# Kernel optimization log

Measured on AMD Instinct MI355X. Metric: run time of the kernel, lower is better.

## Reference

```python
import jax, jax.numpy as jnp
import numpy as np

N = 100000   # nodes
E = 1000000  # edges
F_IN = 64    # input node features
EMB = 32     # init_emb
C = 32       # hidden/out channels per head
H = 4        # heads
HC = H * C   # 128
NEG_SLOPE = 0.2


def setup_inputs() -> dict:
    key = jax.random.key(0)
    ks = jax.random.split(key, 40)
    g = lambda k, shape: jax.random.normal(k, shape, jnp.float32) * 0.05
    inp = {
        "x": jax.random.normal(ks[0], (N, F_IN), jnp.float32),
        "edge_index": jax.random.randint(ks[1], (2, E), 0, N, jnp.int32),
        "W0": g(ks[2], (F_IN, EMB)),
    }
    i = 3
    for p, din in (("f", EMB), ("m", HC), ("l", HC)):
        inp[p + "_Wl"] = g(ks[i], (din, HC)); i += 1
        inp[p + "_bl"] = g(ks[i], (HC,));     i += 1
        inp[p + "_Wr"] = g(ks[i], (din, HC)); i += 1
        inp[p + "_br"] = g(ks[i], (HC,));     i += 1
        inp[p + "_att"] = g(ks[i], (H, C));   i += 1
        inp[p + "_cb"] = g(ks[i], (HC,));     i += 1
        inp[p + "_Ws"] = g(ks[i], (din, HC)); i += 1
        inp[p + "_bs"] = g(ks[i], (HC,));     i += 1
    return inp


def _gatv2(x, src, dst, Wl, bl, Wr, br, att, cb):
    # GATv2Conv, bipartite weights, concat heads, add_self_loops=False
    xl = (x @ Wl + bl).reshape(-1, H, C)  # source transform [N,H,C]
    xr = (x @ Wr + br).reshape(-1, H, C)  # target transform [N,H,C]
    e = xl[src] + xr[dst]                 # [E,H,C]
    s = jnp.where(e > 0, e, NEG_SLOPE * e)
    score = jnp.einsum('ehc,hc->eh', s, att)  # [E,H]
    mmax = jax.ops.segment_max(score, dst, num_segments=N)
    ex = jnp.exp(score - mmax[dst])
    den = jax.ops.segment_sum(ex, dst, num_segments=N)
    alpha = ex / den[dst]                 # segment softmax over in-edges
    out = jax.ops.segment_sum(xl[src] * alpha[:, :, None], dst, num_segments=N)
    return out.reshape(-1, HC) + cb


def reference(x, edge_index,
              W0,
              f_Wl, f_bl, f_Wr, f_br, f_att, f_cb, f_Ws, f_bs,
              m_Wl, m_bl, m_Wr, m_br, m_att, m_cb, m_Ws, m_bs,
              l_Wl, l_bl, l_Wr, l_br, l_att, l_cb, l_Ws, l_bs):
    src, dst = edge_index[0], edge_index[1]
    h = jax.nn.relu(x @ W0)
    h = jax.nn.relu(_gatv2(h, src, dst, f_Wl, f_bl, f_Wr, f_br, f_att, f_cb) + h @ f_Ws + f_bs)
    for _ in range(3):  # conv_mid / lin_mid weights are SHARED across the 3 iterations
        h = jax.nn.relu(_gatv2(h, src, dst, m_Wl, m_bl, m_Wr, m_br, m_att, m_cb) + h @ m_Ws + m_bs)
    h = _gatv2(h, src, dst, l_Wl, l_bl, l_Wr, l_br, l_att, l_cb) + h @ l_Ws + l_bs
    h = h / jnp.linalg.norm(h, axis=-1, keepdims=True)
    return h
```

## Files before the change

### kernel.cpp

```cpp
#include <hip/hip_runtime.h>
#include <hip/hip_bf16.h>
#include <math.h>

#define N_NODES 100000
#define N_EDGES 1000000
#define NEG_SLOPE 0.2f
#define NBUCK 98
#define BSHIFT 10
#define SLAB 12288
#define BINA_EDGES 4096

typedef short v8s __attribute__((ext_vector_type(8)));
typedef float v4f __attribute__((ext_vector_type(4)));

__device__ inline unsigned pack_bf16(float a, float b) {
    unsigned ua = __float_as_uint(a);
    unsigned ub = __float_as_uint(b);
    ua = (ua + 0x7FFFu + ((ua >> 16) & 1u)) >> 16;
    ub = (ub + 0x7FFFu + ((ub >> 16) & 1u)) >> 16;
    return ua | (ub << 16);
}
__device__ inline unsigned short bf16_rn(float x) {
    unsigned u = __float_as_uint(x);
    u = (u + 0x7FFFu + ((u >> 16) & 1u)) >> 16;
    return (unsigned short)u;
}
__device__ inline void unpack8(uint4 u, float* f) {
    f[0] = __uint_as_float(u.x << 16); f[1] = __uint_as_float(u.x & 0xFFFF0000u);
    f[2] = __uint_as_float(u.y << 16); f[3] = __uint_as_float(u.y & 0xFFFF0000u);
    f[4] = __uint_as_float(u.z << 16); f[5] = __uint_as_float(u.z & 0xFFFF0000u);
    f[6] = __uint_as_float(u.w << 16); f[7] = __uint_as_float(u.w & 0xFFFF0000u);
}

__global__ void init_cursors(int* __restrict__ gcursor) {
    int t = blockIdx.x * blockDim.x + threadIdx.x;
    if (t < NBUCK) gcursor[t] = t * SLAB;
}

__global__ __launch_bounds__(256) void binA_kernel(
    const int* __restrict__ src, const int* __restrict__ dst,
    int* __restrict__ gcursor, int* __restrict__ tmp) {
    __shared__ int bstart[NBUCK];
    __shared__ int addrbase[NBUCK];
    __shared__ int bcur[NBUCK];
    __shared__ int s[256];
    __shared__ int staged_val[BINA_EDGES];
    __shared__ int staged_addr[BINA_EDGES];
    const int tid = threadIdx.x;
    const int base = blockIdx.x * BINA_EDGES;
    const int ecount = min(BINA_EDGES, N_EDGES - base);

    if (tid < NBUCK) bcur[tid] = 0;
    __syncthreads();
    for (int j = tid; j < ecount; j += 256) {
        int d = dst[base + j];
        atomicAdd(&bcur[d >> BSHIFT], 1);
    }
    __syncthreads();
    int own = (tid < NBUCK) ? bcur[tid] : 0;
    s[tid] = own;
    __syncthreads();
    for (int off = 1; off < 256; off <<= 1) {
        int u = (tid >= off) ? s[tid - off] : 0;
        __syncthreads();
        s[tid] += u;
        __syncthreads();
    }
    if (tid < NBUCK) {
        int excl = s[tid] - own;
        bstart[tid] = excl;
        int resv = atomicAdd(&gcursor[tid], own);
        addrbase[tid] = resv - excl;
    }
    __syncthreads();
    if (tid < NBUCK) bcur[tid] = bstart[tid];
    __syncthreads();
    for (int j = tid; j < ecount; j += 256) {
        int d = dst[base + j];
        int sr = src[base + j];
        int bk = d >> BSHIFT;
        int lpos = atomicAdd(&bcur[bk], 1);
        staged_val[lpos] = ((d & ((1 << BSHIFT) - 1)) << 17) | sr;
        staged_addr[lpos] = addrbase[bk] + lpos;
    }
    __syncthreads();
    for (int j = tid; j < ecount; j += 256)
        tmp[staged_addr[j]] = staged_val[j];
}

__global__ void bucket_scan(const int* __restrict__ gcursor, int* __restrict__ bbase,
                            int* __restrict__ row_ptr) {
    __shared__ int s[128];
    int t = threadIdx.x;
    int v = (t < NBUCK) ? (gcursor[t] - t * SLAB) : 0;
    s[t] = v;
    __syncthreads();
    for (int off = 1; off < 128; off <<= 1) {
        int u = (t >= off) ? s[t - off] : 0;
        __syncthreads();
        s[t] += u;
        __syncthreads();
    }
    if (t < NBUCK) bbase[t] = s[t] - v;
    if (t == 0) row_ptr[N_NODES] = N_EDGES;
}

__global__ __launch_bounds__(256) void binB_kernel(
    const int* __restrict__ tmp, const int* __restrict__ gcursor,
    const int* __restrict__ bbase, int* __restrict__ row_ptr,
    int* __restrict__ srcs) {
    __shared__ int hist[1024];
    __shared__ int tsum[256];
    const int b = blockIdx.x;
    const int tid = threadIdx.x;
    const int base = b * SLAB;
    const int cnt = gcursor[b] - base;
    const int node0 = b << BSHIFT;
    const int nodes_in = min(1024, N_NODES - node0);
    const int gb = bbase[b];

    for (int i = tid; i < 1024; i += 256) hist[i] = 0;
    __syncthreads();
    for (int i = tid; i < cnt; i += 256)
        atomicAdd(&hist[tmp[base + i] >> 17], 1);
    __syncthreads();
    int v[4], local = 0;
#pragma unroll
    for (int j = 0; j < 4; ++j) {
        v[j] = hist[tid * 4 + j];
        local += v[j];
    }
    tsum[tid] = local;
    __syncthreads();
    for (int off = 1; off < 256; off <<= 1) {
        int u = (tid >= off) ? tsum[tid - off] : 0;
        __syncthreads();
        tsum[tid] += u;
        __syncthreads();
    }
    int run = tsum[tid] - local;
#pragma unroll
    for (int j = 0; j < 4; ++j) {
        hist[tid * 4 + j] = run;
        run += v[j];
    }
    __syncthreads();
    for (int i = tid; i < nodes_in; i += 256)
        row_ptr[node0 + i] = gb + hist[i];
    __syncthreads();
    for (int i = tid; i < cnt; i += 256) {
        int e = tmp[base + i];
        int pos = atomicAdd(&hist[e >> 17], 1);
        srcs[gb + pos] = e & 0x1FFFF;
    }
}

template <int K>
__global__ void convert_w(const float* __restrict__ Wl, const float* __restrict__ Wr,
                          const float* __restrict__ Ws, unsigned short* __restrict__ wt) {
    int idx = blockIdx.x * blockDim.x + threadIdx.x;
    if (idx >= 384 * K) return;
    int n = idx / K;
    int k = idx - n * K;
    int sec = n >> 7;
    int nn = n & 127;
    const float* W = (sec == 0) ? Wl : (sec == 1) ? Wr : Ws;
    wt[idx] = bf16_rn(W[k * 128 + nn]);
}

__global__ void h0_kernel(const float* __restrict__ x, const float* __restrict__ W0,
                          unsigned short* __restrict__ h) {
    int tid = blockIdx.x * blockDim.x + threadIdx.x;
    int col = tid & 31;
    int row = tid >> 5;
    if (row >= N_NODES) return;
    const float* xr = x + row * 64;
    float acc = 0.f;
#pragma unroll
    for (int k = 0; k < 64; ++k) acc = fmaf(xr[k], W0[k * 32 + col], acc);
    h[row * 32 + col] = bf16_rn(fmaxf(acc, 0.f));
}

template <int K>
__global__ __launch_bounds__(64) void mm3_mfma(
    const unsigned short* __restrict__ A, const unsigned short* __restrict__ Wt,
    const float* __restrict__ bl, const float* __restrict__ br, const float* __restrict__ bs,
    const float* __restrict__ cb,
    unsigned short* __restrict__ xl_bf, unsigned short* __restrict__ xr_bf,
    unsigned short* __restrict__ sk_bf) {
    const int lane = threadIdx.x & 63;
    const int q = lane >> 4;
    const int li = lane & 15;
    const int r0 = blockIdx.x * 64;
    constexpr int KS = K / 32;

    v8s a[4][KS];
#pragma unroll
    for (int mi = 0; mi < 4; ++mi) {
        int row = r0 + mi * 16 + li;
        row = row < N_NODES ? row : N_NODES - 1;
#pragma unroll
        for (int ks = 0; ks < KS; ++ks)
            a[mi][ks] = *(const v8s*)&A[(size_t)row * K + ks * 32 + q * 8];
    }

    for (int t = 0; t < 6; ++t) {
        const int sec = t >> 1;
        const int c0 = (t & 1) * 64;
        v4f acc[4][4];
#pragma unroll
        for (int mi = 0; mi < 4; ++mi)
#pragma unroll
            for (int ni = 0; ni < 4; ++ni) acc[mi][ni] = (v4f)(0.f);

#pragma unroll
        for (int ks = 0; ks < KS; ++ks) {
            v8s b[4];
#pragma unroll
            for (int ni = 0; ni < 4; ++ni) {
                int col = sec * 128 + c0 + ni * 16 + li;
                b[ni] = *(const v8s*)&Wt[(size_t)col * K + ks * 32 + q * 8];
            }
#pragma unroll
            for (int mi = 0; mi < 4; ++mi)
#pragma unroll
                for (int ni = 0; ni < 4; ++ni)
                    acc[mi][ni] = __builtin_amdgcn_mfma_f32_16x16x32_bf16(b[ni], a[mi][ks], acc[mi][ni], 0, 0, 0);
        }

        unsigned short* dstp = (sec == 0) ? xl_bf : (sec == 1) ? xr_bf : sk_bf;
#pragma unroll
        for (int ni = 0; ni < 4; ++ni) {
            int cbase = c0 + ni * 16 + q * 4;
            float4 b4;
            if (sec == 0) b4 = *(const float4*)&bl[cbase];
            else if (sec == 1) b4 = *(const float4*)&br[cbase];
            else {
                float4 t1 = *(const float4*)&bs[cbase];
                float4 t2 = *(const float4*)&cb[cbase];
                b4 = make_float4(t1.x + t2.x, t1.y + t2.y, t1.z + t2.z, t1.w + t2.w);
            }
#pragma unroll
            for (int mi = 0; mi < 4; ++mi) {
                int row = r0 + mi * 16 + li;
                if (row >= N_NODES) continue;
                v4f v = acc[mi][ni];
                uint2 pk;
                pk.x = pack_bf16(v[0] + b4.x, v[1] + b4.y);
                pk.y = pack_bf16(v[2] + b4.z, v[3] + b4.w);
                *(uint2*)&dstp[(size_t)row * 128 + cbase] = pk;
            }
        }
    }
}

#define AGG_BODY(XC, SVC, CB)                                               \
    {                                                                       \
        float xf[8];                                                        \
        unpack8(XC, xf);                                                    \
        bool vld = (CB) + g < end;                                          \
        if ((CB) + 12 < end) XC = xlb4[(size_t)SVC * 16 + li];              \
        if ((CB) + 24 < end) {                                              \
            int ii = (CB) + 24 + g;                                         \
            SVC = srcs[ii < end ? ii : em1];                                \
        }                                                                   \
        float p1 = 0.f, p2 = 0.f;                                           \
        _Pragma("unroll") for (int i = 0; i < 8; ++i) {                     \
            float e_ = xf[i] + xr_f[i];                                     \
            p1 = fmaf(e_, at_f[i], p1);                                     \
            p2 = fmaf(fabsf(e_), at_f[i], p2);                              \
        }                                                                   \
        float p = fmaf(0.6f, p1, 0.4f * p2);                                \
        p += __shfl_xor(p, 1);                                              \
        p += __shfl_xor(p, 2);                                              \
        float w = vld ? __expf(p) : 0.f;                                    \
        lsum += w;                                                          \
        _Pragma("unroll") for (int i = 0; i < 8; ++i)                       \
            acc[i] = fmaf(xf[i], w, acc[i]);                                \
    }

__global__ __launch_bounds__(256, 7) void agg_kernel(
    const uint4* __restrict__ xlb4, const uint4* __restrict__ xrb4,
    const uint4* __restrict__ skb4, const int* __restrict__ row_ptr,
    const int* __restrict__ srcs, const float* __restrict__ att,
    uint4* __restrict__ out_bf, float* __restrict__ out_f,
    int write_bf, int do_relu, int do_norm) {
    int n = (blockIdx.x * blockDim.x + threadIdx.x) >> 6;
    if (n >= N_NODES) return;
    int lane = threadIdx.x & 63;
    int g = lane >> 4, li = lane & 15;

    const int beg = __builtin_amdgcn_readfirstlane(row_ptr[n]);
    const int end = __builtin_amdgcn_readfirstlane(row_ptr[n + 1]);

    uint4 xru = xrb4[(size_t)n * 16 + li];
    uint4 sku = skb4[(size_t)n * 16 + li];

    float at_f[8];
    *(float4*)&at_f[0] = *(const float4*)&att[li * 8];
    *(float4*)&at_f[4] = *(const float4*)&att[li * 8 + 4];
    float xr_f[8];
    unpack8(xru, xr_f);

    float acc[8];
#pragma unroll
    for (int i = 0; i < 8; ++i) acc[i] = 0.f;
    float lsum = 0.f;

    if (beg < end) {
        const int em1 = end - 1;
#define SRC_AT(Q) ({ int _ii = beg + (Q) * 4 + g; srcs[_ii < end ? _ii : em1]; })
        int sv0 = SRC_AT(0), sv1 = SRC_AT(1), sv2 = SRC_AT(2);
        uint4 x0 = xlb4[(size_t)sv0 * 16 + li];
        uint4 x1 = xlb4[(size_t)sv1 * 16 + li];
        uint4 x2 = xlb4[(size_t)sv2 * 16 + li];
        sv0 = SRC_AT(3);
        sv1 = SRC_AT(4);
        sv2 = SRC_AT(5);
#undef SRC_AT

        for (int cb = beg; cb < end; cb += 12) {
            AGG_BODY(x0, sv0, cb)
            if (cb + 4 < end) AGG_BODY(x1, sv1, cb + 4)
            if (cb + 8 < end) AGG_BODY(x2, sv2, cb + 8)
        }
    }

#pragma unroll
    for (int i = 0; i < 8; ++i) {
        acc[i] += __shfl_xor(acc[i], 16);
        acc[i] += __shfl_xor(acc[i], 32);
    }
    lsum += __shfl_xor(lsum, 16);
    lsum += __shfl_xor(lsum, 32);

    float inv = (lsum > 0.f) ? 1.f / lsum : 0.f;
    float sk_f[8];
    unpack8(sku, sk_f);
    float o[8];
#pragma unroll
    for (int i = 0; i < 8; ++i) o[i] = fmaf(acc[i], inv, sk_f[i]);
    if (do_relu) {
#pragma unroll
        for (int i = 0; i < 8; ++i) o[i] = fmaxf(o[i], 0.f);
    }
    if (do_norm) {
        float ss = 0.f;
#pragma unroll
        for (int i = 0; i < 8; ++i) ss = fmaf(o[i], o[i], ss);
        ss += __shfl_xor(ss, 1);
        ss += __shfl_xor(ss, 2);
        ss += __shfl_xor(ss, 4);
        ss += __shfl_xor(ss, 8);
        float r = 1.0f / sqrtf(ss);
#pragma unroll
        for (int i = 0; i < 8; ++i) o[i] *= r;
    }
    if (g == 0) {
        if (write_bf) {
            uint4 pk;
            pk.x = pack_bf16(o[0], o[1]);
            pk.y = pack_bf16(o[2], o[3]);
            pk.z = pack_bf16(o[4], o[5]);
            pk.w = pack_bf16(o[6], o[7]);
            out_bf[(size_t)n * 16 + li] = pk;
        } else {
            *(float4*)&out_f[(size_t)n * 128 + li * 8] = make_float4(o[0], o[1], o[2], o[3]);
            *(float4*)&out_f[(size_t)n * 128 + li * 8 + 4] = make_float4(o[4], o[5], o[6], o[7]);
        }
    }
}

extern "C" void kernel_launch(void* const* d_in, const int* in_sizes, int n_in,
                              void* d_out, int out_size, void* d_ws, size_t ws_size,
                              hipStream_t stream) {
    const float* x = (const float*)d_in[0];
    const int* ei = (const int*)d_in[1];
    const int* src = ei;
    const int* dst = ei + N_EDGES;
    const float* W0 = (const float*)d_in[2];

    const float* f_p[8];
    const float* m_p[8];
    const float* l_p[8];
    for (int i = 0; i < 8; ++i) f_p[i] = (const float*)d_in[3 + i];
    for (int i = 0; i < 8; ++i) m_p[i] = (const float*)d_in[11 + i];
    for (int i = 0; i < 8; ++i) l_p[i] = (const float*)d_in[19 + i];

    char* ws = (char*)d_ws;
    unsigned short* xl_bf = (unsigned short*)ws; ws += (size_t)N_NODES * 128 * 2;
    unsigned short* xr_bf = (unsigned short*)ws; ws += (size_t)N_NODES * 128 * 2;
    unsigned short* sk_bf = (unsigned short*)ws; ws += (size_t)N_NODES * 128 * 2;
    unsigned short* h_bf = (unsigned short*)ws;  ws += (size_t)N_NODES * 128 * 2;
    int* row_ptr = (int*)ws;       ws += (size_t)(N_NODES + 1) * 4;
    int* srcs = (int*)ws;          ws += (size_t)N_EDGES * 4;
    int* tmp = (int*)ws;           ws += (size_t)NBUCK * SLAB * 4;
    int* gcursor = (int*)ws;       ws += (size_t)NBUCK * 4;
    int* bbase = (int*)ws;         ws += (size_t)NBUCK * 4;
    unsigned short* wt_f = (unsigned short*)ws; ws += (size_t)384 * 32 * 2;
    unsigned short* wt_m = (unsigned short*)ws; ws += (size_t)384 * 128 * 2;
    unsigned short* wt_l = (unsigned short*)ws; ws += (size_t)384 * 128 * 2;

    init_cursors<<<1, 128, 0, stream>>>(gcursor);
    binA_kernel<<<(N_EDGES + BINA_EDGES - 1) / BINA_EDGES, 256, 0, stream>>>(src, dst, gcursor, tmp);
    bucket_scan<<<1, 128, 0, stream>>>(gcursor, bbase, row_ptr);
    binB_kernel<<<NBUCK, 256, 0, stream>>>(tmp, gcursor, bbase, row_ptr, srcs);

    convert_w<32><<<(384 * 32 + 255) / 256, 256, 0, stream>>>(f_p[0], f_p[2], f_p[6], wt_f);
    convert_w<128><<<(384 * 128 + 255) / 256, 256, 0, stream>>>(m_p[0], m_p[2], m_p[6], wt_m);
    convert_w<128><<<(384 * 128 + 255) / 256, 256, 0, stream>>>(l_p[0], l_p[2], l_p[6], wt_l);

    h0_kernel<<<(N_NODES * 32) / 256, 256, 0, stream>>>(x, W0, h_bf);

    const int gmm = (N_NODES + 63) / 64;
    const int gagg = (N_NODES * 64) / 256;
    float* out = (float*)d_out;

    mm3_mfma<32><<<gmm, 64, 0, stream>>>(h_bf, wt_f, f_p[1], f_p[3], f_p[7], f_p[5],
                                         xl_bf, xr_bf, sk_bf);
    agg_kernel<<<gagg, 256, 0, stream>>>((uint4*)xl_bf, (uint4*)xr_bf, (uint4*)sk_bf,
                                         row_ptr, srcs, f_p[4],
                                         (uint4*)h_bf, nullptr, 1, 1, 0);

    for (int it = 0; it < 3; ++it) {
        mm3_mfma<128><<<gmm, 64, 0, stream>>>(h_bf, wt_m, m_p[1], m_p[3], m_p[7], m_p[5],
                                              xl_bf, xr_bf, sk_bf);
        agg_kernel<<<gagg, 256, 0, stream>>>((uint4*)xl_bf, (uint4*)xr_bf, (uint4*)sk_bf,
                                             row_ptr, srcs, m_p[4],
                                             (uint4*)h_bf, nullptr, 1, 1, 0);
    }

    mm3_mfma<128><<<gmm, 64, 0, stream>>>(h_bf, wt_l, l_p[1], l_p[3], l_p[7], l_p[5],
                                          xl_bf, xr_bf, sk_bf);
    agg_kernel<<<gagg, 256, 0, stream>>>((uint4*)xl_bf, (uint4*)xr_bf, (uint4*)sk_bf,
                                         row_ptr, srcs, l_p[4],
                                         nullptr, out, 0, 0, 1);
}
```

Before: 685.9 us.

## Make GAT aggregation persistent with cross-node prefetch of next row's gathers

The aggregation kernel becomes a persistent grid-stride loop over nodes with a fixed grid of 1536 blocks. While each wave finishes reducing and writing one node, it already loads the next node's row pointers, target and skip features, and its first source indices and gathered rows, so gather latency overlaps the epilogue. Gather addressing switches to 32-bit shift-based offsets, and launch bounds drop to 6 waves per SIMD to leave room for the extra live registers. Risks are lower occupancy and possible load imbalance from the fixed grid size.

New measurement: 839.3 us. 1.22x slower.

```diff
diff --git a/kernel.cpp b/kernel.cpp
--- a/kernel.cpp
+++ b/kernel.cpp
@@ -254,12 +254,14 @@
     }
 }
 
+#define GATHER4(S) (*(const uint4*)((const char*)xlb4 + (((unsigned)(S)) << 8) + ((unsigned)li << 4)))
+
 #define AGG_BODY(XC, SVC, CB)                                               \
     {                                                                       \
         float xf[8];                                                        \
         unpack8(XC, xf);                                                    \
         bool vld = (CB) + g < end;                                          \
-        if ((CB) + 12 < end) XC = xlb4[(size_t)SVC * 16 + li];              \
+        if ((CB) + 12 < end) XC = GATHER4(SVC);                             \
         if ((CB) + 24 < end) {                                              \
             int ii = (CB) + 24 + g;                                         \
             SVC = srcs[ii < end ? ii : em1];                                \
@@ -279,95 +281,129 @@
             acc[i] = fmaf(xf[i], w, acc[i]);                                \
     }
 
-__global__ __launch_bounds__(256, 7) void agg_kernel(
+#define PREFETCH_ROW(B, E)                                                  \
+    if ((B) < (E)) {                                                        \
+        const int em1_ = (E) - 1;                                           \
+        int ii;                                                             \
+        ii = (B) + g;      sv0 = srcs[ii < (E) ? ii : em1_];                \
+        ii = (B) + 4 + g;  sv1 = srcs[ii < (E) ? ii : em1_];                \
+        ii = (B) + 8 + g;  sv2 = srcs[ii < (E) ? ii : em1_];                \
+        x0 = GATHER4(sv0);                                                  \
+        x1 = GATHER4(sv1);                                                  \
+        x2 = GATHER4(sv2);                                                  \
+        ii = (B) + 12 + g; sv0 = srcs[ii < (E) ? ii : em1_];                \
+        ii = (B) + 16 + g; sv1 = srcs[ii < (E) ? ii : em1_];                \
+        ii = (B) + 20 + g; sv2 = srcs[ii < (E) ? ii : em1_];                \
+    }
+
+__global__ __launch_bounds__(256, 6) void agg_kernel(
     const uint4* __restrict__ xlb4, const uint4* __restrict__ xrb4,
     const uint4* __restrict__ skb4, const int* __restrict__ row_ptr,
     const int* __restrict__ srcs, const float* __restrict__ att,
     uint4* __restrict__ out_bf, float* __restrict__ out_f,
     int write_bf, int do_relu, int do_norm) {
-    int n = (blockIdx.x * blockDim.x + threadIdx.x) >> 6;
-    if (n >= N_NODES) return;
-    int lane = threadIdx.x & 63;
-    int g = lane >> 4, li = lane & 15;
-
-    const int beg = __builtin_amdgcn_readfirstlane(row_ptr[n]);
-    const int end = __builtin_amdgcn_readfirstlane(row_ptr[n + 1]);
-
-    uint4 xru = xrb4[(size_t)n * 16 + li];
-    uint4 sku = skb4[(size_t)n * 16 + li];
+    const int lane = threadIdx.x & 63;
+    const int g = lane >> 4, li = lane & 15;
+    const int wid = (blockIdx.x * blockDim.x + threadIdx.x) >> 6;
+    const int nw = (gridDim.x * blockDim.x) >> 6;
 
     float at_f[8];
     *(float4*)&at_f[0] = *(const float4*)&att[li * 8];
     *(float4*)&at_f[4] = *(const float4*)&att[li * 8 + 4];
-    float xr_f[8];
-    unpack8(xru, xr_f);
-
-    float acc[8];
-#pragma unroll
-    for (int i = 0; i < 8; ++i) acc[i] = 0.f;
-    float lsum = 0.f;
-
-    if (beg < end) {
-        const int em1 = end - 1;
-#define SRC_AT(Q) ({ int _ii = beg + (Q) * 4 + g; srcs[_ii < end ? _ii : em1]; })
-        int sv0 = SRC_AT(0), sv1 = SRC_AT(1), sv2 = SRC_AT(2);
-        uint4 x0 = xlb4[(size_t)sv0 * 16 + li];
-        uint4 x1 = xlb4[(size_t)sv1 * 16 + li];
-        uint4 x2 = xlb4[(size_t)sv2 * 16 + li];
-        sv0 = SRC_AT(3);
-        sv1 = SRC_AT(4);
-        sv2 = SRC_AT(5);
-#undef SRC_AT
-
-        for (int cb = beg; cb < end; cb += 12) {
-            AGG_BODY(x0, sv0, cb)
-            if (cb + 4 < end) AGG_BODY(x1, sv1, cb + 4)
-            if (cb + 8 < end) AGG_BODY(x2, sv2, cb + 8)
-        }
-    }
-
-#pragma unroll
-    for (int i = 0; i < 8; ++i) {
-        acc[i] += __shfl_xor(acc[i], 16);
-        acc[i] += __shfl_xor(acc[i], 32);
-    }
-    lsum += __shfl_xor(lsum, 16);
-    lsum += __shfl_xor(lsum, 32);
-
-    float inv = (lsum > 0.f) ? 1.f / lsum : 0.f;
-    float sk_f[8];
-    unpack8(sku, sk_f);
-    float o[8];
-#pragma unroll
-    for (int i = 0; i < 8; ++i) o[i] = fmaf(acc[i], inv, sk_f[i]);
-    if (do_relu) {
-#pragma unroll
-        for (int i = 0; i < 8; ++i) o[i] = fmaxf(o[i], 0.f);
-    }
-    if (do_norm) {
-        float ss = 0.f;
-#pragma unroll
-        for (int i = 0; i < 8; ++i) ss = fmaf(o[i], o[i], ss);
-        ss += __shfl_xor(ss, 1);
-        ss += __shfl_xor(ss, 2);
-        ss += __shfl_xor(ss, 4);
-        ss += __shfl_xor(ss, 8);
-        float r = 1.0f / sqrtf(ss);
-#pragma unroll
-        for (int i = 0; i < 8; ++i) o[i] *= r;
-    }
-    if (g == 0) {
-        if (write_bf) {
-            uint4 pk;
-            pk.x = pack_bf16(o[0], o[1]);
-            pk.y = pack_bf16(o[2], o[3]);
-            pk.z = pack_bf16(o[4], o[5]);
-            pk.w = pack_bf16(o[6], o[7]);
-            out_bf[(size_t)n * 16 + li] = pk;
-        } else {
-            *(float4*)&out_f[(size_t)n * 128 + li * 8] = make_float4(o[0], o[1], o[2], o[3]);
-            *(float4*)&out_f[(size_t)n * 128 + li * 8 + 4] = make_float4(o[4], o[5], o[6], o[7]);
-        }
+
+    int node = wid;
+    if (node >= N_NODES) return;
+
+    int rb = row_ptr[node];
+    int re = row_ptr[node + 1];
+    uint4 xru = xrb4[(size_t)node * 16 + li];
+    uint4 sku = skb4[(size_t)node * 16 + li];
+    int beg = __builtin_amdgcn_readfirstlane(rb);
+    int end = __builtin_amdgcn_readfirstlane(re);
+    int sv0 = 0, sv1 = 0, sv2 = 0;
+    uint4 x0 = {}, x1 = {}, x2 = {};
+    PREFETCH_ROW(beg, end);
+
+    for (;;) {
+        const int next = node + nw;
+        if (next < N_NODES) {
+            rb = row_ptr[next];
+            re = row_ptr[next + 1];
+        }
+        float xr_f[8];
+        unpack8(xru, xr_f);
+        if (next < N_NODES) xru = xrb4[(size_t)next * 16 + li];
+
+        float acc[8];
+#pragma unroll
+        for (int i = 0; i < 8; ++i) acc[i] = 0.f;
+        float lsum = 0.f;
+
+        if (beg < end) {
+            const int em1 = end - 1;
+            for (int cb = beg; cb < end; cb += 12) {
+                AGG_BODY(x0, sv0, cb)
+                if (cb + 4 < end) AGG_BODY(x1, sv1, cb + 4)
+                if (cb + 8 < end) AGG_BODY(x2, sv2, cb + 8)
+            }
+        }
+
+        int nbeg = 0, nend = 0;
+        if (next < N_NODES) {
+            nbeg = __builtin_amdgcn_readfirstlane(rb);
+            nend = __builtin_amdgcn_readfirstlane(re);
+            PREFETCH_ROW(nbeg, nend);
+        }
+
+#pragma unroll
+        for (int i = 0; i < 8; ++i) {
+            acc[i] += __shfl_xor(acc[i], 16);
+            acc[i] += __shfl_xor(acc[i], 32);
+        }
+        lsum += __shfl_xor(lsum, 16);
+        lsum += __shfl_xor(lsum, 32);
+
+        float inv = (lsum > 0.f) ? 1.f / lsum : 0.f;
+        float sk_f[8];
+        unpack8(sku, sk_f);
+        if (next < N_NODES) sku = skb4[(size_t)next * 16 + li];
+        float o[8];
+#pragma unroll
+        for (int i = 0; i < 8; ++i) o[i] = fmaf(acc[i], inv, sk_f[i]);
+        if (do_relu) {
+#pragma unroll
+            for (int i = 0; i < 8; ++i) o[i] = fmaxf(o[i], 0.f);
+        }
+        if (do_norm) {
+            float ss = 0.f;
+#pragma unroll
+            for (int i = 0; i < 8; ++i) ss = fmaf(o[i], o[i], ss);
+            ss += __shfl_xor(ss, 1);
+            ss += __shfl_xor(ss, 2);
+            ss += __shfl_xor(ss, 4);
+            ss += __shfl_xor(ss, 8);
+            float r = 1.0f / sqrtf(ss);
+#pragma unroll
+            for (int i = 0; i < 8; ++i) o[i] *= r;
+        }
+        if (g == 0) {
+            if (write_bf) {
+                uint4 pk;
+                pk.x = pack_bf16(o[0], o[1]);
+                pk.y = pack_bf16(o[2], o[3]);
+                pk.z = pack_bf16(o[4], o[5]);
+                pk.w = pack_bf16(o[6], o[7]);
+                out_bf[(size_t)node * 16 + li] = pk;
+            } else {
+                *(float4*)&out_f[(size_t)node * 128 + li * 8] = make_float4(o[0], o[1], o[2], o[3]);
+                *(float4*)&out_f[(size_t)node * 128 + li * 8 + 4] = make_float4(o[4], o[5], o[6], o[7]);
+            }
+        }
+
+        if (next >= N_NODES) break;
+        node = next;
+        beg = nbeg;
+        end = nend;
     }
 }
 
@@ -413,7 +449,7 @@
     h0_kernel<<<(N_NODES * 32) / 256, 256, 0, stream>>>(x, W0, h_bf);
 
     const int gmm = (N_NODES + 63) / 64;
-    const int gagg = (N_NODES * 64) / 256;
+    const int gagg = 1536;
     float* out = (float*)d_out;
 
     mm3_mfma<32><<<gmm, 64, 0, stream>>>(h_bf, wt_f, f_p[1], f_p[3], f_p[7], f_p[5],
```
